# Performance work log

Hardware: AMD Instinct MI355X
Metric: run time of the kernel (lower is better)

The kernel has to match this reference:

```python
import jax, jax.numpy as jnp
import numpy as np

# sizes / constants (mirroring the source module's constants)
M, T_SOL, NX, NY = 12, 64, 256, 256
N_TIMES, NOUT = 50, 256
LX, LY_TARGET = 60.0, 75.0
C_CU_TARGET, C_NI_TARGET = 0.001, 0.0001
T_MAX = 200.0
SIGMA, H, DH = 0.25, 4, 8


def setup_inputs() -> dict:
    key = jax.random.key(0)
    ks = jax.random.split(key, 7)
    u = jax.random.uniform(ks[0], (M, 3), dtype=jnp.float32)
    # rows: (Ly in [30,120], c_Cu in [0,0.0029], c_Ni in [0,0.0018])
    params = jnp.stack([30.0 + 90.0 * u[:, 0], 0.0029 * u[:, 1], 0.0018 * u[:, 2]], axis=1)
    c1_src = jax.random.uniform(ks[1], (M, T_SOL, NX, NY), dtype=jnp.float32) * 0.003
    c2_src = jax.random.uniform(ks[2], (M, T_SOL, NX, NY), dtype=jnp.float32) * 0.002
    Wq = jax.random.normal(ks[3], (H * DH, 3), dtype=jnp.float32) * 0.5
    bq = jax.random.normal(ks[4], (H * DH,), dtype=jnp.float32) * 0.1
    Wk = jax.random.normal(ks[5], (H * DH, 3), dtype=jnp.float32) * 0.5
    bk = jax.random.normal(ks[6], (H * DH,), dtype=jnp.float32) * 0.1
    return {"params": params, "c1_src": c1_src, "c2_src": c2_src,
            "Wq": Wq, "bq": bq, "Wk": Wk, "bk": bk}


def _bilinear_resample(xs, ys, vals, xq, yq):
    """RegularGridInterpolator(linear, fill_value=0) on grid (xs[NX], ys[NY]).
    vals: [T, NX, NY]; query is the outer-product grid xq[PX] x yq[PY].
    Separable bilinear -> [T, PX, PY]."""
    ix = jnp.clip(jnp.searchsorted(xs, xq, side='right') - 1, 0, xs.shape[0] - 2)
    tx = (xq - xs[ix]) / (xs[ix + 1] - xs[ix])
    vx = vals[:, ix, :] * (1.0 - tx)[None, :, None] + vals[:, ix + 1, :] * tx[None, :, None]
    iy = jnp.clip(jnp.searchsorted(ys, yq, side='right') - 1, 0, ys.shape[0] - 2)
    ty = (yq - ys[iy]) / (ys[iy + 1] - ys[iy])
    out = vx[:, :, iy] * (1.0 - ty)[None, None, :] + vx[:, :, iy + 1] * ty[None, None, :]
    inb = ((xq >= xs[0]) & (xq <= xs[-1]))[:, None] & ((yq >= ys[0]) & (yq <= ys[-1]))[None, :]
    return jnp.where(inb[None], out, jnp.float32(0.0))


def _forward(params, c1_src, c2_src, Wq, bq, Wk, bk):
    lys, c_cus, c_nis = params[:, 0], params[:, 1], params[:, 2]
    ly_n = (lys - 30.0) / 90.0
    ccu_n = c_cus / 0.0029
    cni_n = c_nis / 0.0018
    p = jnp.stack([ly_n, ccu_n, cni_n], axis=1)                      # [M,3]
    t = jnp.array([[(LY_TARGET - 30.0) / 90.0,
                    C_CU_TARGET / 0.0029,
                    C_NI_TARGET / 0.0018]], dtype=params.dtype)       # [1,3]
    Q = (t @ Wq.T + bq).reshape(1, H, DH)
    K = (p @ Wk.T + bk).reshape(-1, H, DH)
    attn = jnp.einsum('nhd,mhd->nmh', K, Q) / (DH ** 0.5)            # [M,1,H]
    attn_w = jax.nn.softmax(attn, axis=0).mean(axis=2)[:, 0]         # [M]
    dist2 = (((ly_n - t[0, 0]) / SIGMA) ** 2
             + ((ccu_n - t[0, 1]) / SIGMA) ** 2
             + ((cni_n - t[0, 2]) / SIGMA) ** 2)
    sw = jnp.exp(-dist2 / 2.0)
    sw = sw / sw.sum()
    w = attn_w * sw
    w = w / w.sum()                                                  # [M]

    # grids: source x shared; per-solution y grid rescaled to [0, LY_TARGET]
    xs = jnp.linspace(0.0, LX, NX)
    ys_scaled = (jnp.linspace(0.0, 1.0, NY)[None, :] * lys[:, None]) * (LY_TARGET / lys)[:, None]  # [M,NY]
    xq = jnp.linspace(0.0, LX, NOUT)
    yq = jnp.linspace(0.0, LY_TARGET, NOUT)

    times = jnp.linspace(0.0, min(T_MAX, T_MAX), N_TIMES)
    tidx = jnp.clip((times / T_MAX * T_SOL).astype(jnp.int32), 0, T_SOL - 1)  # [T]
    c1_sel = c1_src[:, tidx]                                          # [M,T,NX,NY]
    c2_sel = c2_src[:, tidx]

    res1, res2 = jax.vmap(
        lambda ys, v1, v2: (_bilinear_resample(xs, ys, v1, xq, yq),
                            _bilinear_resample(xs, ys, v2, xq, yq))
    )(ys_scaled, c1_sel, c2_sel)                                      # each [M,T,NOUT,NOUT]

    c1 = jnp.einsum('m,mtij->tij', w, res1)
    c2 = jnp.einsum('m,mtij->tij', w, res2)
    c1 = c1.at[:, :, 0].set(C_CU_TARGET)
    c2 = c2.at[:, :, -1].set(C_NI_TARGET)
    return jnp.stack([c1, c2])                                        # [2,T,NOUT,NOUT]


def reference(params, c1_src, c2_src, Wq, bq, Wk, bk):
    return _forward(params, c1_src, c2_src, Wq, bq, Wk, bk)
```

## Files before the change

kernel.cpp:

```cpp
#include <hip/hip_runtime.h>

#define MM    12
#define TSOL  64
#define NXX   256
#define NYY   256
#define NTT   50
#define NOUTT 256
#define IPB   2

__device__ int   g_iy[MM * NOUTT];
__device__ float g_w0[MM * NOUTT];
__device__ float g_w1[MM * NOUTT];

__global__ __launch_bounds__(256) void ai_setup_kernel(
    const float* __restrict__ params,
    const float* __restrict__ Wq, const float* __restrict__ bq,
    const float* __restrict__ Wk, const float* __restrict__ bk)
{
    const int k = threadIdx.x;
    const int m = blockIdx.x;

    __shared__ float s_attn[MM][4];
    __shared__ float s_sw[MM];
    __shared__ float s_wm;
    __shared__ float s_ys[NYY];

    if (k < MM) {
        float ly = params[k * 3 + 0];
        float p0 = (ly - 30.0f) / 90.0f;
        float p1 = params[k * 3 + 1] / 0.0029f;
        float p2 = params[k * 3 + 2] / 0.0018f;
        const float t0 = 0.5f;
        const float t1 = 0.001f / 0.0029f;
        const float t2 = 0.0001f / 0.0018f;
        for (int h = 0; h < 4; ++h) {
            float acc = 0.0f;
            for (int d = 0; d < 8; ++d) {
                int o = h * 8 + d;
                float q  = t0 * Wq[o * 3 + 0] + t1 * Wq[o * 3 + 1] + t2 * Wq[o * 3 + 2] + bq[o];
                float kv = p0 * Wk[o * 3 + 0] + p1 * Wk[o * 3 + 1] + p2 * Wk[o * 3 + 2] + bk[o];
                acc += kv * q;
            }
            s_attn[k][h] = acc * 0.35355339059327373f;
        }
        float d0 = (p0 - t0) / 0.25f;
        float d1 = (p1 - t1) / 0.25f;
        float d2 = (p2 - t2) / 0.25f;
        s_sw[k] = expf(-(d0 * d0 + d1 * d1 + d2 * d2) * 0.5f);
    }
    __syncthreads();

    if (k == 0) {
        float aw[MM];
        for (int j = 0; j < MM; ++j) aw[j] = 0.0f;
        for (int h = 0; h < 4; ++h) {
            float mx = s_attn[0][h];
            for (int j = 1; j < MM; ++j) mx = fmaxf(mx, s_attn[j][h]);
            float e[MM]; float sum = 0.0f;
            for (int j = 0; j < MM; ++j) { e[j] = expf(s_attn[j][h] - mx); sum += e[j]; }
            for (int j = 0; j < MM; ++j) aw[j] += e[j] / sum;
        }
        float swsum = 0.0f;
        for (int j = 0; j < MM; ++j) swsum += s_sw[j];
        float wj[MM]; float wsum = 0.0f;
        for (int j = 0; j < MM; ++j) {
            wj[j] = (aw[j] * 0.25f) * (s_sw[j] / swsum);
            wsum += wj[j];
        }
        s_wm = wj[m] / wsum;
    }

    {
        float ly  = params[m * 3 + 0];
        float inv = 75.0f / ly;
        float l01 = (float)k * (1.0f / 255.0f);
        s_ys[k] = (l01 * ly) * inv;
    }
    __syncthreads();

    float w  = s_wm;
    float yq = (float)k * (75.0f / 255.0f);
    int l = 0, r = NYY;
    while (l < r) { int mid = (l + r) >> 1; if (s_ys[mid] <= yq) l = mid + 1; else r = mid; }
    int iy = l - 1;
    iy = iy < 0 ? 0 : (iy > NYY - 2 ? NYY - 2 : iy);
    float ty  = (yq - s_ys[iy]) / (s_ys[iy + 1] - s_ys[iy]);
    bool  inb = (yq >= s_ys[0]) && (yq <= s_ys[NYY - 1]);
    g_iy[m * NOUTT + k] = iy;
    g_w0[m * NOUTT + k] = inb ? w * (1.0f - ty) : 0.0f;
    g_w1[m * NOUTT + k] = inb ? w * ty : 0.0f;
}

__global__ __launch_bounds__(256) void ai_resample_kernel(
    const float* __restrict__ c1, const float* __restrict__ c2,
    float* __restrict__ out)
{
    __shared__ float s_rows[IPB * 24 * NYY];

    const int tid  = threadIdx.x;
    const int lane = tid & 63;
    const int wv   = tid >> 6;
    const int t    = blockIdx.y;
    const int i0   = blockIdx.x * IPB;
    int tsrc = (t * TSOL) / (NTT - 1);
    if (tsrc > TSOL - 1) tsrc = TSOL - 1;

    int   iy[MM]; float w0[MM], w1[MM];
#pragma unroll
    for (int m = 0; m < MM; ++m) {
        iy[m] = g_iy[m * NOUTT + tid];
        w0[m] = g_w0[m * NOUTT + tid];
        w1[m] = g_w1[m * NOUTT + tid];
    }

#pragma unroll
    for (int s = 0; s < IPB * 24 / 4; ++s) {
        int rs  = s * 4 + wv;
        int r   = rs / 24;
        int row = rs % 24;
        int ch  = row / 12;
        int m   = row % 12;
        const float* src = ch ? c2 : c1;
        size_t gbase = ((size_t)(m * TSOL + tsrc) * NXX + (size_t)(i0 + r)) * NYY;
        const float* gp = src + gbase + (size_t)lane * 4;
        float* lp = &s_rows[rs * NYY];
        __builtin_amdgcn_global_load_lds(
            (const __attribute__((address_space(1))) void*)gp,
            (__attribute__((address_space(3))) void*)lp,
            16, 0, 0);
    }
    __syncthreads();

#pragma unroll
    for (int r = 0; r < IPB; ++r) {
        const float* rowset = &s_rows[r * 24 * NYY];
        float acc1 = 0.0f, acc2 = 0.0f;
#pragma unroll
        for (int m = 0; m < MM; ++m) {
            const float* r1 = rowset + m * NYY;
            const float* r2 = rowset + (12 + m) * NYY;
            int j = iy[m];
            float a0 = r1[j], a1 = r1[j + 1];
            float b0 = r2[j], b1 = r2[j + 1];
            acc1 += w0[m] * a0 + w1[m] * a1;
            acc2 += w0[m] * b0 + w1[m] * b1;
        }
        int i = i0 + r;
        float o1 = (tid == 0)         ? 0.001f  : acc1;
        float o2 = (tid == NOUTT - 1) ? 0.0001f : acc2;
        out[((size_t)t * NOUTT + (size_t)i) * NOUTT + (size_t)tid] = o1;
        out[((size_t)(NTT + t) * NOUTT + (size_t)i) * NOUTT + (size_t)tid] = o2;
    }
}

extern "C" void kernel_launch(void* const* d_in, const int* in_sizes, int n_in,
                              void* d_out, int out_size, void* d_ws, size_t ws_size,
                              hipStream_t stream) {
    const float* params = (const float*)d_in[0];
    const float* c1     = (const float*)d_in[1];
    const float* c2     = (const float*)d_in[2];
    const float* Wq     = (const float*)d_in[3];
    const float* bq     = (const float*)d_in[4];
    const float* Wk     = (const float*)d_in[5];
    const float* bk     = (const float*)d_in[6];
    float* out = (float*)d_out;

    ai_setup_kernel<<<dim3(MM), dim3(256), 0, stream>>>(params, Wq, bq, Wk, bk);
    ai_resample_kernel<<<dim3(NOUTT / IPB, NTT), dim3(256), 0, stream>>>(c1, c2, out);
}
```

Measured before the change: 404.6 us.

## Gather resample inputs directly from global memory, drop LDS staging

The resample kernel no longer stages source rows into LDS with global_load_lds and a barrier. Each thread now gathers its two bilinear neighbours for all 12 solutions straight from global memory, using precomputed 32-bit row offsets. The y-interpolation table is packed into one float4 per entry so it loads in a single vector read, and each block now handles 4 output rows instead of 2. The aim is to cut LDS traffic and barrier stalls and to raise occupancy, at the cost of scattered, partly uncoalesced global gathers that rely on cache reuse across threads.

```diff
diff --git a/kernel.cpp b/kernel.cpp
--- a/kernel.cpp
+++ b/kernel.cpp
@@ -6,11 +6,9 @@
 #define NYY   256
 #define NTT   50
 #define NOUTT 256
-#define IPB   2
+#define IPB   4
 
-__device__ int   g_iy[MM * NOUTT];
-__device__ float g_w0[MM * NOUTT];
-__device__ float g_w1[MM * NOUTT];
+__device__ float4 g_tab[MM * NOUTT];
 
 __global__ __launch_bounds__(256) void ai_setup_kernel(
     const float* __restrict__ params,
@@ -86,62 +84,47 @@
     iy = iy < 0 ? 0 : (iy > NYY - 2 ? NYY - 2 : iy);
     float ty  = (yq - s_ys[iy]) / (s_ys[iy + 1] - s_ys[iy]);
     bool  inb = (yq >= s_ys[0]) && (yq <= s_ys[NYY - 1]);
-    g_iy[m * NOUTT + k] = iy;
-    g_w0[m * NOUTT + k] = inb ? w * (1.0f - ty) : 0.0f;
-    g_w1[m * NOUTT + k] = inb ? w * ty : 0.0f;
+    float4 tb;
+    tb.x = inb ? w * (1.0f - ty) : 0.0f;
+    tb.y = inb ? w * ty          : 0.0f;
+    tb.z = __int_as_float(iy);
+    tb.w = 0.0f;
+    g_tab[m * NOUTT + k] = tb;
 }
 
 __global__ __launch_bounds__(256) void ai_resample_kernel(
     const float* __restrict__ c1, const float* __restrict__ c2,
     float* __restrict__ out)
 {
-    __shared__ float s_rows[IPB * 24 * NYY];
-
-    const int tid  = threadIdx.x;
-    const int lane = tid & 63;
-    const int wv   = tid >> 6;
-    const int t    = blockIdx.y;
-    const int i0   = blockIdx.x * IPB;
+    const int tid = threadIdx.x;
+    const int t   = blockIdx.y;
+    const int i0  = blockIdx.x * IPB;
     int tsrc = (t * TSOL) / (NTT - 1);
     if (tsrc > TSOL - 1) tsrc = TSOL - 1;
 
-    int   iy[MM]; float w0[MM], w1[MM];
+    float w0[MM], w1[MM];
+    unsigned int iy[MM];
 #pragma unroll
     for (int m = 0; m < MM; ++m) {
-        iy[m] = g_iy[m * NOUTT + tid];
-        w0[m] = g_w0[m * NOUTT + tid];
-        w1[m] = g_w1[m * NOUTT + tid];
+        float4 tb = g_tab[m * NOUTT + tid];
+        w0[m] = tb.x;
+        w1[m] = tb.y;
+        iy[m] = (unsigned int)__float_as_int(tb.z);
     }
 
+    unsigned int rbase[MM];
 #pragma unroll
-    for (int s = 0; s < IPB * 24 / 4; ++s) {
-        int rs  = s * 4 + wv;
-        int r   = rs / 24;
-        int row = rs % 24;
-        int ch  = row / 12;
-        int m   = row % 12;
-        const float* src = ch ? c2 : c1;
-        size_t gbase = ((size_t)(m * TSOL + tsrc) * NXX + (size_t)(i0 + r)) * NYY;
-        const float* gp = src + gbase + (size_t)lane * 4;
-        float* lp = &s_rows[rs * NYY];
-        __builtin_amdgcn_global_load_lds(
-            (const __attribute__((address_space(1))) void*)gp,
-            (__attribute__((address_space(3))) void*)lp,
-            16, 0, 0);
-    }
-    __syncthreads();
+    for (int m = 0; m < MM; ++m)
+        rbase[m] = (((unsigned int)(m * TSOL + tsrc) * NXX) + (unsigned int)i0) * NYY + iy[m];
 
-#pragma unroll
+#pragma unroll 2
     for (int r = 0; r < IPB; ++r) {
-        const float* rowset = &s_rows[r * 24 * NYY];
         float acc1 = 0.0f, acc2 = 0.0f;
 #pragma unroll
         for (int m = 0; m < MM; ++m) {
-            const float* r1 = rowset + m * NYY;
-            const float* r2 = rowset + (12 + m) * NYY;
-            int j = iy[m];
-            float a0 = r1[j], a1 = r1[j + 1];
-            float b0 = r2[j], b1 = r2[j + 1];
+            unsigned int off = rbase[m] + (unsigned int)r * NYY;
+            float a0 = c1[off], a1 = c1[off + 1];
+            float b0 = c2[off], b1 = c2[off + 1];
             acc1 += w0[m] * a0 + w1[m] * a1;
             acc2 += w0[m] * b0 + w1[m] * b1;
         }
```

After: 427.7 us. 5.7% more time.
